# Kernel optimization log

Hardware: AMD Instinct MI355X
Metric: run time of the kernel (lower is better)

The kernel has to match this reference:

```python
import jax, jax.numpy as jnp
import numpy as np

L, D, H, FF, V = 8, 768, 8, 2048, 32000
MAXLEN, TMAX = 512, 4
S = MAXLEN * TMAX  # 2048 context length
HD = D // H
EPS = 1e-4  # layer_norm_eps from module defaults


def setup_inputs() -> dict:
    key = jax.random.key(0)
    ks = jax.random.split(key, 16)
    s = 0.02
    B = 1
    rn = lambda k, shape: jax.random.normal(k, shape, jnp.float32) * s
    # sinusoidal positional encoding over MAXLEN real-token positions
    pos = np.arange(MAXLEN)[:, None]
    div = np.exp(np.arange(0, D, 2) * (-np.log(10000.0) / D))
    pe = np.zeros((MAXLEN, D), np.float32)
    pe[:, 0::2] = np.sin(pos * div)
    pe[:, 1::2] = np.cos(pos * div)
    return {
        "state_embeddings": jax.random.normal(ks[0], (B, S, D), jnp.float32),
        "padding_mask": jnp.zeros((B, S), bool),
        "pe": jnp.asarray(pe),
        "thought_emb": rn(ks[1], (TMAX, D)),
        "w_qkv": rn(ks[2], (L, 3 * D, D)),
        "b_qkv": jnp.zeros((L, 3 * D), jnp.float32),
        "w_out": rn(ks[3], (L, D, D)),
        "b_out": jnp.zeros((L, D), jnp.float32),
        "ln1_g": jnp.ones((L, D), jnp.float32),
        "ln1_b": jnp.zeros((L, D), jnp.float32),
        "ln2_g": jnp.ones((L, D), jnp.float32),
        "ln2_b": jnp.zeros((L, D), jnp.float32),
        "w_ff1": rn(ks[4], (L, FF, D)),
        "b_ff1": jnp.zeros((L, FF), jnp.float32),
        "w_ff2": rn(ks[5], (L, D, FF)),
        "b_ff2": jnp.zeros((L, D), jnp.float32),
        "fn_g": jnp.ones((D,), jnp.float32),
        "fn_b": jnp.zeros((D,), jnp.float32),
        "w_policy": rn(ks[6], (V, D)),
        "w_v1": rn(ks[7], (FF, D)),
        "b_v1": jnp.zeros((FF,), jnp.float32),
        "w_v2": rn(ks[8], (1, FF)),
        "b_v2": jnp.zeros((1,), jnp.float32),
        "n_thoughts_taken": 3,
    }


def _layer_norm(x, g, b):
    m = x.mean(-1, keepdims=True)
    v = ((x - m) ** 2).mean(-1, keepdims=True)
    return (x - m) / jnp.sqrt(v + EPS) * g + b


def reference(state_embeddings, padding_mask, pe, thought_emb, w_qkv, b_qkv, w_out, b_out, ln1_g, ln1_b, ln2_g, ln2_b, w_ff1, b_ff1, w_ff2, b_ff2, fn_g, fn_b, w_policy, w_v1, b_v1, w_v2, b_v2, n_thoughts_taken):
    tt = int(n_thoughts_taken)
    T = tt + 1  # block size (token + thoughts taken)
    B = state_embeddings.shape[0]
    R = MAXLEN  # real_token_count: all token slots real (no padding)
    # --- DualPositionalEncoding ---
    x = state_embeddings[:, :MAXLEN * T].reshape(B, MAXLEN, T, D)
    x = x + pe[None, :, None, :] + thought_emb[None, None, :T, :]
    x = x.reshape(B, MAXLEN * T, D)
    x = jnp.pad(x, ((0, 0), (0, S - MAXLEN * T), (0, 0)))
    # --- ThoughtsFormer block-causal mask (keep=True means attend) ---
    i = jnp.arange(S)
    tok, off = i // T, i % T
    same_block = (tok[:, None] == tok[None, :]) & (off[:, None] >= off[None, :]) & (tok[:, None] < R)
    global_cols = (off[None, :] == 0) & (tok[None, :] < R) & (i[:, None] > i[None, :]) & (i[:, None] < R * T)
    keep = (same_block | global_cols)[None, None] & (~padding_mask)[:, None, None, :]
    scale = 1.0 / np.sqrt(HD)

    def layer(h, p):
        wq, bq, wo, bo, g1, b1, g2, b2, wf1, bf1, wf2, bf2 = p
        # pre-norm self-attention
        y = _layer_norm(h, g1, b1)
        q, k, v = jnp.split(y @ wq.T + bq, 3, axis=-1)
        q = q.reshape(B, S, H, HD)
        k = k.reshape(B, S, H, HD)
        v = v.reshape(B, S, H, HD)
        scores = jnp.einsum('bihd,bjhd->bhij', q, k) * scale
        attn = jax.nn.softmax(jnp.where(keep, scores, -jnp.inf), axis=-1)
        o = jnp.einsum('bhij,bjhd->bihd', attn, v).reshape(B, S, D)
        h = h + o @ wo.T + bo
        # pre-norm FFN with exact (erf) GELU
        y = _layer_norm(h, g2, b2)
        h = h + jax.nn.gelu(y @ wf1.T + bf1, approximate=False) @ wf2.T + bf2
        h = jnp.where(jnp.isnan(h), 0.0, h)
        return h, None

    x, _ = jax.lax.scan(layer, x, (w_qkv, b_qkv, w_out, b_out, ln1_g, ln1_b, ln2_g, ln2_b, w_ff1, b_ff1, w_ff2, b_ff2))
    x = _layer_norm(x, fn_g, fn_b)  # TransformerEncoder final norm
    logits = x @ w_policy.T  # policy head (no bias)
    values = jax.nn.gelu(x @ w_v1.T + b_v1, approximate=False) @ w_v2.T + b_v2
    return logits, values
```

## Files before the change

kernel.cpp:

```cpp
#include <hip/hip_runtime.h>
#include <math.h>

#define S_TOT 2048
#define DMODEL 768
#define QKVD 2304
#define NHEAD 8
#define HDIM 96
#define FFDIM 2048
#define VOCAB 32000
#define MAXLEN_C 512
#define POL_CHUNK 3200
#define VLT_LD 2080
#define NEG_BIG (-3.0e38f)
#define M_INIT (-1.0e30f)
#define QK_SCALE 0.10206207261596575f

typedef __bf16 bf16x8 __attribute__((ext_vector_type(8)));
typedef float f32x4 __attribute__((ext_vector_type(4)));
typedef unsigned short u16x8 __attribute__((ext_vector_type(8)));
typedef unsigned short u16x4 __attribute__((ext_vector_type(4)));

__device__ __forceinline__ float gelu_exact(float x) {
  return 0.5f * x * (1.0f + erff(x * 0.70710678118654752f));
}

__device__ __forceinline__ float bf2f(unsigned short u) {
  union { unsigned int i; float f; } v;
  v.i = ((unsigned int)u) << 16;
  return v.f;
}

__device__ __forceinline__ unsigned short f2bf(float f) {
  union { float f; unsigned int i; } v;
  v.f = f;
  unsigned int x = v.i;
  return (unsigned short)((x + 0x7fffu + ((x >> 16) & 1u)) >> 16);
}

__device__ __forceinline__ unsigned int pack2bf(float a, float b) {
  return (unsigned int)f2bf(a) | ((unsigned int)f2bf(b) << 16);
}

__device__ __forceinline__ void gload_lds16(const unsigned short* g, unsigned short* l) {
  __builtin_amdgcn_global_load_lds(
      (const __attribute__((address_space(1))) unsigned int*)g,
      (__attribute__((address_space(3))) unsigned int*)l, 16, 0, 0);
}

__global__ __launch_bounds__(256) void embed_kernel(
    const float* __restrict__ se, const float* __restrict__ pe,
    const float* __restrict__ th, const int* __restrict__ ntt,
    float* __restrict__ X) {
  int idx = blockIdx.x * 256 + threadIdx.x;
  if (idx >= S_TOT * DMODEL) return;
  int p = idx / DMODEL;
  int d = idx - p * DMODEL;
  int T = ntt[0] + 1;
  float v = 0.0f;
  if (p < MAXLEN_C * T) {
    v = se[idx] + pe[(p / T) * DMODEL + d] + th[(p % T) * DMODEL + d];
  }
  X[idx] = v;
}

__global__ __launch_bounds__(256) void ln_bf_kernel(
    const float* __restrict__ X, const float* __restrict__ g,
    const float* __restrict__ b, unsigned short* __restrict__ Y) {
  __shared__ float red[4];
  const int row = blockIdx.x;
  const int tid = threadIdx.x;
  const float* x = X + (size_t)row * DMODEL;
  float v0 = x[tid], v1 = x[tid + 256], v2 = x[tid + 512];
  float s = v0 + v1 + v2;
  for (int o = 32; o; o >>= 1) s += __shfl_xor(s, o);
  if ((tid & 63) == 0) red[tid >> 6] = s;
  __syncthreads();
  float mean = (red[0] + red[1] + red[2] + red[3]) * (1.0f / DMODEL);
  float d0 = v0 - mean, d1 = v1 - mean, d2 = v2 - mean;
  float s2 = d0 * d0 + d1 * d1 + d2 * d2;
  for (int o = 32; o; o >>= 1) s2 += __shfl_xor(s2, o);
  __syncthreads();
  if ((tid & 63) == 0) red[tid >> 6] = s2;
  __syncthreads();
  float var = (red[0] + red[1] + red[2] + red[3]) * (1.0f / DMODEL);
  float rstd = rsqrtf(var + 1e-4f);
  unsigned short* y = Y + (size_t)row * DMODEL;
  y[tid]       = f2bf(d0 * rstd * g[tid]       + b[tid]);
  y[tid + 256] = f2bf(d1 * rstd * g[tid + 256] + b[tid + 256]);
  y[tid + 512] = f2bf(d2 * rstd * g[tid + 512] + b[tid + 512]);
}

__global__ __launch_bounds__(256) void cvt_kernel(
    const float* __restrict__ s, unsigned short* __restrict__ d, int n) {
  int i = (blockIdx.x * 256 + threadIdx.x) * 4;
  if (i >= n) return;
  float4 v = *(const float4*)(s + i);
  u16x4 o;
  o[0] = f2bf(v.x); o[1] = f2bf(v.y); o[2] = f2bf(v.z); o[3] = f2bf(v.w);
  *(u16x4*)(d + i) = o;
}

__global__ __launch_bounds__(256) void cvt4_kernel(
    const float* __restrict__ s0, const float* __restrict__ s1,
    const float* __restrict__ s2, const float* __restrict__ s3,
    unsigned short* __restrict__ d0, unsigned short* __restrict__ d1,
    unsigned short* __restrict__ d2, unsigned short* __restrict__ d3,
    int n0, int n1, int n2, int n3) {
  int i = (blockIdx.x * 256 + threadIdx.x) * 4;
  const float* s;
  unsigned short* d;
  if (i < n0) { s = s0; d = d0; }
  else if (i < n0 + n1) { i -= n0; s = s1; d = d1; }
  else if (i < n0 + n1 + n2) { i -= n0 + n1; s = s2; d = d2; }
  else if (i < n0 + n1 + n2 + n3) { i -= n0 + n1 + n2; s = s3; d = d3; }
  else return;
  float4 v = *(const float4*)(s + i);
  u16x4 o;
  o[0] = f2bf(v.x); o[1] = f2bf(v.y); o[2] = f2bf(v.z); o[3] = f2bf(v.w);
  *(u16x4*)(d + i) = o;
}

__global__ __launch_bounds__(256) void cvt6_kernel(
    const float* __restrict__ s0, const float* __restrict__ s1,
    const float* __restrict__ s2, const float* __restrict__ s3,
    const float* __restrict__ s4, const float* __restrict__ s5,
    unsigned short* __restrict__ d0, unsigned short* __restrict__ d1,
    unsigned short* __restrict__ d2, unsigned short* __restrict__ d3,
    unsigned short* __restrict__ d4, unsigned short* __restrict__ d5,
    int n0, int n1, int n2, int n3, int n4, int n5) {
  int i = (blockIdx.x * 256 + threadIdx.x) * 4;
  const float* s;
  unsigned short* d;
  if (i < n0) { s = s0; d = d0; }
  else if (i < n0 + n1) { i -= n0; s = s1; d = d1; }
  else if (i < n0 + n1 + n2) { i -= n0 + n1; s = s2; d = d2; }
  else if (i < n0 + n1 + n2 + n3) { i -= n0 + n1 + n2; s = s3; d = d3; }
  else if (i < n0 + n1 + n2 + n3 + n4) { i -= n0 + n1 + n2 + n3; s = s4; d = d4; }
  else if (i < n0 + n1 + n2 + n3 + n4 + n5) { i -= n0 + n1 + n2 + n3 + n4; s = s5; d = d5; }
  else return;
  float4 v = *(const float4*)(s + i);
  u16x4 o;
  o[0] = f2bf(v.x); o[1] = f2bf(v.y); o[2] = f2bf(v.z); o[3] = f2bf(v.w);
  *(u16x4*)(d + i) = o;
}

__global__ __launch_bounds__(256) void gemm_bf16_kernel(
    const unsigned short* __restrict__ A, const unsigned short* __restrict__ B,
    const float* __restrict__ bias, const float* __restrict__ res,
    void* __restrict__ Cout, int M, int N, int K, int ldc, int act, int outbf,
    int swiz) {
  __shared__ __align__(16) unsigned short As[3 * 4096];
  __shared__ __align__(16) unsigned short Bs[3 * 4096];
  const int t = threadIdx.x;
  const int w = t >> 6, l = t & 63;
  int n_blk, m_blk;
  if (swiz) {
    const int g = blockIdx.x;
    const int chunk = gridDim.x >> 3;
    const int logical = (g & 7) * chunk + (g >> 3);
    m_blk = logical & 15;
    n_blk = logical >> 4;
  } else {
    n_blk = blockIdx.x; m_blk = blockIdx.y;
  }
  const int n0 = n_blk * 128, i0 = m_blk * 128;
  const int wr = w >> 1, wc = w & 1;
  const int lr = l & 15;
  const int koff = (l >> 4) * 8;

  f32x4 acc[4][4] = {};

  const int srow = t >> 2;
  const int scol = (t & 3) * 8;
  const unsigned short* Ag = A + (size_t)(i0 + srow) * K + scol;
  const unsigned short* Bg = B + (size_t)(n0 + srow) * K + scol;
  const int lo0 = (w << 9);
  const int lo1 = 2048 + (w << 9);

#define STAGE128(buf, k0)                                        \
  do {                                                           \
    gload_lds16(Ag + (k0), &As[(buf) * 4096 + lo0]);             \
    gload_lds16(Ag + (size_t)64 * K + (k0), &As[(buf) * 4096 + lo1]); \
    gload_lds16(Bg + (k0), &Bs[(buf) * 4096 + lo0]);             \
    gload_lds16(Bg + (size_t)64 * K + (k0), &Bs[(buf) * 4096 + lo1]); \
  } while (0)

#define COMPUTE128(buf)                                                   \
  do {                                                                    \
    const unsigned short* Ab = &As[(buf) * 4096];                         \
    const unsigned short* Bb = &Bs[(buf) * 4096];                         \
    bf16x8 af[4], bfr[4];                                                 \
    _Pragma("unroll") for (int fi = 0; fi < 4; ++fi)                      \
        af[fi] = *(const bf16x8*)&Ab[(wr * 64 + fi * 16 + lr) * 32 + koff]; \
    _Pragma("unroll") for (int fj = 0; fj < 4; ++fj)                      \
        bfr[fj] = *(const bf16x8*)&Bb[(wc * 64 + fj * 16 + lr) * 32 + koff]; \
    _Pragma("unroll") for (int fi = 0; fi < 4; ++fi)                      \
      _Pragma("unroll") for (int fj = 0; fj < 4; ++fj)                    \
          acc[fi][fj] = __builtin_amdgcn_mfma_f32_16x16x32_bf16(          \
              bfr[fj], af[fi], acc[fi][fj], 0, 0, 0);                     \
  } while (0)

  const int nt = K >> 5;
  STAGE128(0, 0);
  if (nt > 1) STAGE128(1, 32);
  for (int tt = 0; tt < nt; ++tt) {
    const int cb = tt % 3;
    if (tt + 2 < nt) {
      STAGE128((tt + 2) % 3, (tt + 2) << 5);
      asm volatile("s_waitcnt vmcnt(8)" ::: "memory");
    } else if (tt + 1 < nt) {
      asm volatile("s_waitcnt vmcnt(4)" ::: "memory");
    } else {
      asm volatile("s_waitcnt vmcnt(0)" ::: "memory");
    }
    __builtin_amdgcn_s_barrier();
    __builtin_amdgcn_sched_barrier(0);
    COMPUTE128(cb);
    __builtin_amdgcn_sched_barrier(0);
    __builtin_amdgcn_s_barrier();
  }

  const int mloc = l & 15, ng = (l >> 4) * 4;
#pragma unroll
  for (int fi = 0; fi < 4; ++fi) {
    const int i = i0 + wr * 64 + fi * 16 + mloc;
    const size_t rowbase = (size_t)i * ldc;
#pragma unroll
    for (int fj = 0; fj < 4; ++fj) {
      const int nb = n0 + wc * 64 + fj * 16 + ng;
      float z0 = acc[fi][fj][0], z1 = acc[fi][fj][1];
      float z2 = acc[fi][fj][2], z3 = acc[fi][fj][3];
      if (bias) {
        float4 bv = *(const float4*)(bias + nb);
        z0 += bv.x; z1 += bv.y; z2 += bv.z; z3 += bv.w;
      }
      if (act) {
        z0 = gelu_exact(z0); z1 = gelu_exact(z1);
        z2 = gelu_exact(z2); z3 = gelu_exact(z3);
      }
      if (res) {
        float4 rv = *(const float4*)(res + rowbase + nb);
        z0 += rv.x; z1 += rv.y; z2 += rv.z; z3 += rv.w;
      }
      if (outbf) {
        u16x4 o;
        o[0] = f2bf(z0); o[1] = f2bf(z1); o[2] = f2bf(z2); o[3] = f2bf(z3);
        *(u16x4*)((unsigned short*)Cout + rowbase + nb) = o;
      } else {
        *(float4*)((float*)Cout + rowbase + nb) = make_float4(z0, z1, z2, z3);
      }
    }
  }
#undef STAGE128
#undef COMPUTE128
}

__global__ __launch_bounds__(512) void gemm256_bf16_kernel(
    const unsigned short* __restrict__ A, const unsigned short* __restrict__ B,
    void* __restrict__ Cout, int M, int N, int K, int ldc) {
  __shared__ __align__(16) unsigned short As[2 * 8192];
  __shared__ __align__(16) unsigned short Bs[2 * 4096];
  const int t = threadIdx.x;
  const int w = t >> 6, l = t & 63;
  const int g = blockIdx.x;
  const int chunk = gridDim.x >> 3;
  const int logical = (g & 7) * chunk + (g >> 3);
  const int m_blk = logical & 7;
  const int n_blk = logical >> 3;
  const int n0 = n_blk * 128, i0 = m_blk * 256;
  const int wr = w >> 1;
  const int wc = w & 1;
  const int lr = l & 15;
  const int koff = (l >> 4) * 8;

  f32x4 acc[4][4] = {};

  const int srow = t >> 2;
  const int scol = (t & 3) * 8;
  const unsigned short* Ag = A + (size_t)(i0 + srow) * K + scol;
  const unsigned short* Bg = B + (size_t)(n0 + srow) * K + scol;
  const int lo = (w << 9);

#define STAGE256(buf, k0)                                             \
  do {                                                                \
    gload_lds16(Ag + (k0), &As[(buf) * 8192 + lo]);                   \
    gload_lds16(Ag + (size_t)128 * K + (k0), &As[(buf) * 8192 + 4096 + lo]); \
    gload_lds16(Bg + (k0), &Bs[(buf) * 4096 + lo]);                   \
  } while (0)

  const int nt = K >> 5;
  STAGE256(0, 0);
  for (int tt = 0; tt < nt; ++tt) {
    const int cb = tt & 1;
    if (tt + 1 < nt) {
      STAGE256(cb ^ 1, (tt + 1) << 5);
      asm volatile("s_waitcnt vmcnt(3)" ::: "memory");
    } else {
      asm volatile("s_waitcnt vmcnt(0)" ::: "memory");
    }
    __builtin_amdgcn_s_barrier();
    __builtin_amdgcn_sched_barrier(0);
    {
      const unsigned short* Ab = &As[cb * 8192];
      const unsigned short* Bb = &Bs[cb * 4096];
      bf16x8 af[4], bfr[4];
#pragma unroll
      for (int fi = 0; fi < 4; ++fi)
        af[fi] = *(const bf16x8*)&Ab[(wr * 64 + fi * 16 + lr) * 32 + koff];
#pragma unroll
      for (int fj = 0; fj < 4; ++fj)
        bfr[fj] = *(const bf16x8*)&Bb[(wc * 64 + fj * 16 + lr) * 32 + koff];
#pragma unroll
      for (int fi = 0; fi < 4; ++fi)
#pragma unroll
        for (int fj = 0; fj < 4; ++fj)
          acc[fi][fj] = __builtin_amdgcn_mfma_f32_16x16x32_bf16(
              bfr[fj], af[fi], acc[fi][fj], 0, 0, 0);
    }
    __builtin_amdgcn_sched_barrier(0);
    __builtin_amdgcn_s_barrier();
  }

  const int mloc = l & 15, ng = (l >> 4) * 4;
#pragma unroll
  for (int fi = 0; fi < 4; ++fi) {
    const int i = i0 + wr * 64 + fi * 16 + mloc;
    const size_t rowbase = (size_t)i * ldc;
#pragma unroll
    for (int fj = 0; fj < 4; ++fj) {
      const int nb = n0 + wc * 64 + fj * 16 + ng;
      *(float4*)((float*)Cout + rowbase + nb) =
          make_float4(acc[fi][fj][0], acc[fi][fj][1], acc[fi][fj][2], acc[fi][fj][3]);
    }
  }
#undef STAGE256
}

__global__ __launch_bounds__(256) void gemm64_bf16_kernel(
    const unsigned short* __restrict__ A, const unsigned short* __restrict__ B,
    const float* __restrict__ bias, const float* __restrict__ res,
    void* __restrict__ Cout, int M, int N, int K, int ldc, int act, int outbf) {
  __shared__ __align__(16) unsigned short As[3 * 4096];
  __shared__ __align__(16) unsigned short Bs[3 * 4096];
  const int t = threadIdx.x;
  const int w = t >> 6, l = t & 63;
  const int n0 = blockIdx.x * 64, i0 = blockIdx.y * 64;
  const int wr = w >> 1, wc = w & 1;
  const int lr = l & 15;
  const int koff = (l >> 4) * 8;

  f32x4 acc[2][2] = {};

  const int srow = t >> 2;
  const int scol = (t & 3) * 8;
  const unsigned short* Ag = A + (size_t)(i0 + srow) * K + scol;
  const unsigned short* Bg = B + (size_t)(n0 + srow) * K + scol;
  const int lo0 = (w << 9);
  const int lo1 = 2048 + (w << 9);

#define STAGE64(buf, k0)                                      \
  do {                                                        \
    gload_lds16(Ag + (k0), &As[(buf) * 4096 + lo0]);          \
    gload_lds16(Ag + (k0) + 32, &As[(buf) * 4096 + lo1]);     \
    gload_lds16(Bg + (k0), &Bs[(buf) * 4096 + lo0]);          \
    gload_lds16(Bg + (k0) + 32, &Bs[(buf) * 4096 + lo1]);     \
  } while (0)

#define COMPUTE64(buf)                                                        \
  do {                                                                        \
    const unsigned short* Ab = &As[(buf) * 4096];                             \
    const unsigned short* Bb = &Bs[(buf) * 4096];                             \
    bf16x8 af[2][2], bfr[2][2];                                               \
    _Pragma("unroll") for (int fi = 0; fi < 2; ++fi)                          \
      _Pragma("unroll") for (int kk = 0; kk < 2; ++kk)                        \
          af[fi][kk] = *(const bf16x8*)&Ab[kk * 2048 + (wr * 32 + fi * 16 + lr) * 32 + koff]; \
    _Pragma("unroll") for (int fj = 0; fj < 2; ++fj)                          \
      _Pragma("unroll") for (int kk = 0; kk < 2; ++kk)                        \
          bfr[fj][kk] = *(const bf16x8*)&Bb[kk * 2048 + (wc * 32 + fj * 16 + lr) * 32 + koff]; \
    _Pragma("unroll") for (int fi = 0; fi < 2; ++fi)                          \
      _Pragma("unroll") for (int fj = 0; fj < 2; ++fj)                        \
        _Pragma("unroll") for (int kk = 0; kk < 2; ++kk)                      \
            acc[fi][fj] = __builtin_amdgcn_mfma_f32_16x16x32_bf16(            \
                bfr[fj][kk], af[fi][kk], acc[fi][fj], 0, 0, 0);               \
  } while (0)

  const int nt = K >> 6;
  STAGE64(0, 0);
  if (nt > 1) STAGE64(1, 64);
  for (int tt = 0; tt < nt; ++tt) {
    const int cb = tt % 3;
    if (tt + 2 < nt) {
      STAGE64((tt + 2) % 3, (tt + 2) << 6);
      asm volatile("s_waitcnt vmcnt(8)" ::: "memory");
    } else if (tt + 1 < nt) {
      asm volatile("s_waitcnt vmcnt(4)" ::: "memory");
    } else {
      asm volatile("s_waitcnt vmcnt(0)" ::: "memory");
    }
    __builtin_amdgcn_s_barrier();
    __builtin_amdgcn_sched_barrier(0);
    COMPUTE64(cb);
    __builtin_amdgcn_sched_barrier(0);
    __builtin_amdgcn_s_barrier();
  }

  const int mloc = l & 15, ng = (l >> 4) * 4;
#pragma unroll
  for (int fi = 0; fi < 2; ++fi) {
    const int i = i0 + wr * 32 + fi * 16 + mloc;
    const size_t rowbase = (size_t)i * ldc;
#pragma unroll
    for (int fj = 0; fj < 2; ++fj) {
      const int nb = n0 + wc * 32 + fj * 16 + ng;
      float z0 = acc[fi][fj][0], z1 = acc[fi][fj][1];
      float z2 = acc[fi][fj][2], z3 = acc[fi][fj][3];
      if (bias) {
        float4 bv = *(const float4*)(bias + nb);
        z0 += bv.x; z1 += bv.y; z2 += bv.z; z3 += bv.w;
      }
      if (act) {
        z0 = gelu_exact(z0); z1 = gelu_exact(z1);
        z2 = gelu_exact(z2); z3 = gelu_exact(z3);
      }
      if (res) {
        float4 rv = *(const float4*)(res + rowbase + nb);
        z0 += rv.x; z1 += rv.y; z2 += rv.z; z3 += rv.w;
      }
      if (outbf) {
        u16x4 o;
        o[0] = f2bf(z0); o[1] = f2bf(z1); o[2] = f2bf(z2); o[3] = f2bf(z3);
        *(u16x4*)((unsigned short*)Cout + rowbase + nb) = o;
      } else {
        *(float4*)((float*)Cout + rowbase + nb) = make_float4(z0, z1, z2, z3);
      }
    }
  }
#undef STAGE64
#undef COMPUTE64
}

__global__ __launch_bounds__(256) void repack_kernel(
    const unsigned short* __restrict__ qkv, const int* __restrict__ ntt,
    unsigned short* __restrict__ Kg, unsigned short* __restrict__ Vgt,
    unsigned short* __restrict__ Vlt) {
  __shared__ unsigned short vt[64][104];
  const int pb = blockIdx.x * 64, h = blockIdx.y;
  const int T = ntt[0] + 1;
  const int tid = threadIdx.x;

  for (int idx = tid; idx < 64 * 96; idx += 256) {
    int pp = idx / 96, d = idx - pp * 96;
    vt[pp][d] = qkv[(size_t)(pb + pp) * QKVD + 2 * DMODEL + h * HDIM + d];
  }
  const int firstpp = (T - pb % T) % T;
  const int ng = (64 - firstpp + T - 1) / T;
  for (int idx = tid; idx < ng * 96; idx += 256) {
    int gi = idx / 96, d = idx - gi * 96;
    int p = pb + firstpp + gi * T;
    int g = p / T;
    if (g < MAXLEN_C)
      Kg[((size_t)h * 512 + g) * 96 + d] = qkv[(size_t)p * QKVD + DMODEL + h * HDIM + d];
  }
  __syncthreads();
  for (int idx = tid; idx < 96 * 64; idx += 256) {
    int d = idx >> 6, pp = idx & 63;
    Vlt[((size_t)h * 96 + d) * VLT_LD + pb + pp] = vt[pp][d];
  }
  for (int idx = tid; idx < ng * 96; idx += 256) {
    int d = idx / ng, gi = idx - d * ng;
    int pp = firstpp + gi * T;
    int g = (pb + pp) / T;
    if (g < MAXLEN_C && d < 96)
      Vgt[((size_t)h * 96 + d) * 512 + g] = vt[pp][d];
  }
}

__global__ __launch_bounds__(256) void attn_flash_kernel(
    const unsigned short* __restrict__ qkv, const unsigned short* __restrict__ Kg,
    const unsigned short* __restrict__ Vgt, const unsigned short* __restrict__ Vlt,
    const int* __restrict__ ntt, unsigned short* __restrict__ att) {
  __shared__ float Osh[4][96][17];
  __shared__ float Msh[4][16];
  __shared__ float Lsh[4][16];
  const int s = blockIdx.x, h = blockIdx.y;
  const int T = ntt[0] + 1;
  const int tid = threadIdx.x;
  const int w = tid >> 6, l = tid & 63;
  const int q15 = l & 15, grp = l >> 4;
  const int p0 = s * 16;
  const int p = p0 + q15;
  const int myTok = p / T;

  const unsigned short* qrow = qkv + (size_t)p * QKVD + h * HDIM + grp * 8;
  bf16x8 qf0 = *(const bf16x8*)(qrow);
  bf16x8 qf1 = *(const bf16x8*)(qrow + 32);
  bf16x8 qf2 = *(const bf16x8*)(qrow + 64);

  float m_run = M_INIT, l_run = 0.0f;
  f32x4 oacc[6] = {};

  const int gmax = (p0 + 15) / T;
  const int KP = (gmax >> 5) + 1;
  const unsigned short* KgH = Kg + (size_t)h * 512 * 96;
  const unsigned short* VgH = Vgt + (size_t)h * 96 * 512;

  for (int kp = w; kp < KP; kp += 4) {
    f32x4 s0 = {}, s1 = {};
    const unsigned short* k0r = KgH + (size_t)(kp * 32 + q15) * 96 + grp * 8;
    const unsigned short* k1r = k0r + 16 * 96;
    {
      bf16x8 a0 = *(const bf16x8*)(k0r);
      bf16x8 a1 = *(const bf16x8*)(k1r);
      bf16x8 b0 = *(const bf16x8*)(k0r + 32);
      bf16x8 b1 = *(const bf16x8*)(k1r + 32);
      bf16x8 c0 = *(const bf16x8*)(k0r + 64);
      bf16x8 c1 = *(const bf16x8*)(k1r + 64);
      __builtin_amdgcn_s_setprio(1);
      s0 = __builtin_amdgcn_mfma_f32_16x16x32_bf16(a0, qf0, s0, 0, 0, 0);
      s1 = __builtin_amdgcn_mfma_f32_16x16x32_bf16(a1, qf0, s1, 0, 0, 0);
      s0 = __builtin_amdgcn_mfma_f32_16x16x32_bf16(b0, qf1, s0, 0, 0, 0);
      s1 = __builtin_amdgcn_mfma_f32_16x16x32_bf16(b1, qf1, s1, 0, 0, 0);
      s0 = __builtin_amdgcn_mfma_f32_16x16x32_bf16(c0, qf2, s0, 0, 0, 0);
      s1 = __builtin_amdgcn_mfma_f32_16x16x32_bf16(c1, qf2, s1, 0, 0, 0);
      __builtin_amdgcn_s_setprio(0);
    }
    float sc[8];
#pragma unroll
    for (int e = 0; e < 4; ++e) {
      int g = kp * 32 + grp * 4 + e;
      sc[e] = (g * T <= p) ? s0[e] * QK_SCALE : NEG_BIG;
      g += 16;
      sc[4 + e] = (g * T <= p) ? s1[e] * QK_SCALE : NEG_BIG;
    }
    float tmax = sc[0];
#pragma unroll
    for (int e = 1; e < 8; ++e) tmax = fmaxf(tmax, sc[e]);
    tmax = fmaxf(tmax, __shfl_xor(tmax, 16));
    tmax = fmaxf(tmax, __shfl_xor(tmax, 32));
    float mnew = fmaxf(m_run, tmax);
    float alpha = __expf(m_run - mnew);
    float pv[8], ps = 0.0f;
#pragma unroll
    for (int e = 0; e < 8; ++e) { pv[e] = __expf(sc[e] - mnew); ps += pv[e]; }
    ps += __shfl_xor(ps, 16);
    ps += __shfl_xor(ps, 32);
    l_run = l_run * alpha + ps;
    m_run = mnew;
#pragma unroll
    for (int dt = 0; dt < 6; ++dt) oacc[dt] *= alpha;
    unsigned int pk0[2], pk1[2];
    pk0[0] = pack2bf(pv[0], pv[1]); pk0[1] = pack2bf(pv[2], pv[3]);
    pk1[0] = pack2bf(pv[4], pv[5]); pk1[1] = pack2bf(pv[6], pv[7]);
    union { unsigned int u[4]; bf16x8 v; } pf;
#pragma unroll
    for (int w2 = 0; w2 < 4; ++w2) {
      int src = (((grp & 1) << 1) + (w2 >> 1)) * 16 + q15;
      int y0 = __shfl((int)pk0[w2 & 1], src);
      int y1 = __shfl((int)pk1[w2 & 1], src);
      pf.u[w2] = (grp >> 1) ? (unsigned int)y1 : (unsigned int)y0;
    }
    __builtin_amdgcn_s_setprio(1);
#pragma unroll
    for (int dt = 0; dt < 6; ++dt) {
      bf16x8 vf = *(const bf16x8*)(VgH + (size_t)(dt * 16 + q15) * 512 + kp * 32 + grp * 8);
      oacc[dt] = __builtin_amdgcn_mfma_f32_16x16x32_bf16(vf, pf.v, oacc[dt], 0, 0, 0);
    }
    __builtin_amdgcn_s_setprio(0);
  }

  if (w == 3) {
    f32x4 s0 = {};
    const unsigned short* kl = qkv + (size_t)(p0 + q15) * QKVD + DMODEL + h * HDIM + grp * 8;
    __builtin_amdgcn_s_setprio(1);
    s0 = __builtin_amdgcn_mfma_f32_16x16x32_bf16(*(const bf16x8*)(kl), qf0, s0, 0, 0, 0);
    s0 = __builtin_amdgcn_mfma_f32_16x16x32_bf16(*(const bf16x8*)(kl + 32), qf1, s0, 0, 0, 0);
    s0 = __builtin_amdgcn_mfma_f32_16x16x32_bf16(*(const bf16x8*)(kl + 64), qf2, s0, 0, 0, 0);
    __builtin_amdgcn_s_setprio(0);
    float sc[4];
#pragma unroll
    for (int e = 0; e < 4; ++e) {
      int pk = p0 + grp * 4 + e;
      bool ok = (pk / T == myTok) && (pk % T != 0) && (pk <= p);
      sc[e] = ok ? s0[e] * QK_SCALE : NEG_BIG;
    }
    float tmax = fmaxf(fmaxf(sc[0], sc[1]), fmaxf(sc[2], sc[3]));
    tmax = fmaxf(tmax, __shfl_xor(tmax, 16));
    tmax = fmaxf(tmax, __shfl_xor(tmax, 32));
    float mnew = fmaxf(m_run, tmax);
    float alpha = __expf(m_run - mnew);
    float pv[4], ps = 0.0f;
#pragma unroll
    for (int e = 0; e < 4; ++e) { pv[e] = __expf(sc[e] - mnew); ps += pv[e]; }
    ps += __shfl_xor(ps, 16);
    ps += __shfl_xor(ps, 32);
    l_run = l_run * alpha + ps;
    m_run = mnew;
#pragma unroll
    for (int dt = 0; dt < 6; ++dt) oacc[dt] *= alpha;
    unsigned int pk0[2];
    pk0[0] = pack2bf(pv[0], pv[1]); pk0[1] = pack2bf(pv[2], pv[3]);
    union { unsigned int u[4]; bf16x8 v; } pf;
#pragma unroll
    for (int w2 = 0; w2 < 4; ++w2) {
      int src = (((grp & 1) << 1) + (w2 >> 1)) * 16 + q15;
      int y0 = __shfl((int)pk0[w2 & 1], src);
      pf.u[w2] = (grp >> 1) ? 0u : (unsigned int)y0;
    }
    __builtin_amdgcn_s_setprio(1);
#pragma unroll
    for (int dt = 0; dt < 6; ++dt) {
      bf16x8 vf = *(const bf16x8*)(Vlt + ((size_t)h * 96 + dt * 16 + q15) * VLT_LD + p0 + grp * 8);
      oacc[dt] = __builtin_amdgcn_mfma_f32_16x16x32_bf16(vf, pf.v, oacc[dt], 0, 0, 0);
    }
    __builtin_amdgcn_s_setprio(0);
  }

  if (l < 16) { Msh[w][l] = m_run; Lsh[w][l] = l_run; }
#pragma unroll
  for (int dt = 0; dt < 6; ++dt)
#pragma unroll
    for (int e = 0; e < 4; ++e)
      Osh[w][dt * 16 + grp * 4 + e][q15] = oacc[dt][e];
  __syncthreads();

  {
    const int q = tid & 15, dg = tid >> 4;
    float m0 = Msh[0][q], m1 = Msh[1][q], m2 = Msh[2][q], m3 = Msh[3][q];
    float ms = fmaxf(fmaxf(m0, m1), fmaxf(m2, m3));
    float c0 = __expf(m0 - ms), c1 = __expf(m1 - ms);
    float c2 = __expf(m2 - ms), c3 = __expf(m3 - ms);
    float lsum = c0 * Lsh[0][q] + c1 * Lsh[1][q] + c2 * Lsh[2][q] + c3 * Lsh[3][q];
    float rinv = 1.0f / lsum;
    unsigned short* orow = att + (size_t)(p0 + q) * DMODEL + h * HDIM;
#pragma unroll
    for (int j = 0; j < 6; ++j) {
      int d = dg * 6 + j;
      float o = c0 * Osh[0][d][q] + c1 * Osh[1][d][q] +
                c2 * Osh[2][d][q] + c3 * Osh[3][d][q];
      orow[d] = f2bf(o * rinv);
    }
  }
}

__global__ __launch_bounds__(256) void v2_kernel(
    const unsigned short* __restrict__ F1, const float* __restrict__ w2,
    const float* __restrict__ b2, float* __restrict__ out) {
  __shared__ float red[4];
  const int row = blockIdx.x;
  const int tid = threadIdx.x;
  float s = 0.0f;
  const unsigned short* xr = F1 + (size_t)row * FFDIM;
  for (int f = tid; f < FFDIM; f += 256) s += bf2f(xr[f]) * w2[f];
  for (int o = 32; o; o >>= 1) s += __shfl_xor(s, o);
  if ((tid & 63) == 0) red[tid >> 6] = s;
  __syncthreads();
  if (tid == 0) out[row] = red[0] + red[1] + red[2] + red[3] + b2[0];
}

extern "C" void kernel_launch(void* const* d_in, const int* in_sizes, int n_in,
                              void* d_out, int out_size, void* d_ws, size_t ws_size,
                              hipStream_t stream) {
  const float* se      = (const float*)d_in[0];
  const float* pe      = (const float*)d_in[2];
  const float* th      = (const float*)d_in[3];
  const float* w_qkv   = (const float*)d_in[4];
  const float* b_qkv   = (const float*)d_in[5];
  const float* w_out   = (const float*)d_in[6];
  const float* b_out   = (const float*)d_in[7];
  const float* ln1_g   = (const float*)d_in[8];
  const float* ln1_b   = (const float*)d_in[9];
  const float* ln2_g   = (const float*)d_in[10];
  const float* ln2_b   = (const float*)d_in[11];
  const float* w_ff1   = (const float*)d_in[12];
  const float* b_ff1   = (const float*)d_in[13];
  const float* w_ff2   = (const float*)d_in[14];
  const float* b_ff2   = (const float*)d_in[15];
  const float* fn_g    = (const float*)d_in[16];
  const float* fn_b    = (const float*)d_in[17];
  const float* w_pol   = (const float*)d_in[18];
  const float* w_v1    = (const float*)d_in[19];
  const float* b_v1    = (const float*)d_in[20];
  const float* w_v2    = (const float*)d_in[21];
  const float* b_v2    = (const float*)d_in[22];
  const int*   ntt     = (const int*)d_in[23];

  float* logits = (float*)d_out;
  float* values = logits + (size_t)S_TOT * VOCAB;

  const int nq = 3 * DMODEL * DMODEL, no = DMODEL * DMODEL;
  const int nf1 = FFDIM * DMODEL, nf2 = DMODEL * FFDIM;
  const int npol = VOCAB * DMODEL;

  char* p = (char*)d_ws;
  float* X             = (float*)p;          p += (size_t)S_TOT * DMODEL * 4;
  unsigned short* Ybf  = (unsigned short*)p; p += (size_t)S_TOT * DMODEL * 2;
  unsigned short* QKVb = (unsigned short*)p; p += (size_t)S_TOT * QKVD * 2;
  unsigned short* ATTb = (unsigned short*)p; p += (size_t)S_TOT * DMODEL * 2;
  unsigned short* F1b  = (unsigned short*)p; p += (size_t)S_TOT * FFDIM * 2;
  unsigned short* Kg   = (unsigned short*)p; p += (size_t)NHEAD * 512 * 96 * 2;
  unsigned short* Vgt  = (unsigned short*)p; p += (size_t)NHEAD * 96 * 512 * 2;
  unsigned short* Vlt  = (unsigned short*)p; p += (size_t)NHEAD * 96 * VLT_LD * 2;

  const size_t wbytes = ((size_t)8 * (nq + no + nf1 + nf2) + npol + nf1) * 2;
  const size_t used   = (size_t)(p - (char*)d_ws);
  const bool bigws = ws_size >= used + wbytes + (1u << 20);

  unsigned short *WqA, *WoA, *Wf1A, *Wf2A, *WpolA, *Wv1A;
  if (bigws) {
    WqA   = (unsigned short*)p; p += (size_t)8 * nq * 2;
    WoA   = (unsigned short*)p; p += (size_t)8 * no * 2;
    Wf1A  = (unsigned short*)p; p += (size_t)8 * nf1 * 2;
    Wf2A  = (unsigned short*)p; p += (size_t)8 * nf2 * 2;
    WpolA = (unsigned short*)p; p += (size_t)npol * 2;
    Wv1A  = (unsigned short*)p;
  } else {
    WqA   = (unsigned short*)p; p += (size_t)nq * 2;
    WoA   = (unsigned short*)p; p += (size_t)no * 2;
    Wf1A  = (unsigned short*)p; p += (size_t)nf1 * 2;
    Wf2A  = (unsigned short*)p; p += (size_t)nf2 * 2;
    WpolA = (unsigned short*)p;
    Wv1A  = Wf1A;
  }

  dim3 blk(256);

  if (bigws) {
    const int t0 = 8 * nq, t1 = 8 * no, t2 = 8 * nf1, t3 = 8 * nf2;
    const long total = (long)t0 + t1 + t2 + t3 + npol + nf1;
    cvt6_kernel<<<dim3((unsigned)((total / 4 + 255) / 256)), blk, 0, stream>>>(
        w_qkv, w_out, w_ff1, w_ff2, w_pol, w_v1,
        WqA, WoA, Wf1A, Wf2A, WpolA, Wv1A,
        t0, t1, t2, t3, npol, nf1);
  }

  embed_kernel<<<dim3((S_TOT * DMODEL + 255) / 256), blk, 0, stream>>>(se, pe, th, ntt, X);

  for (int l = 0; l < 8; ++l) {
    const unsigned short* pWq  = bigws ? WqA  + (size_t)l * nq  : WqA;
    const unsigned short* pWo  = bigws ? WoA  + (size_t)l * no  : WoA;
    const unsigned short* pWf1 = bigws ? Wf1A + (size_t)l * nf1 : Wf1A;
    const unsigned short* pWf2 = bigws ? Wf2A + (size_t)l * nf2 : Wf2A;
    if (!bigws) {
      const int ncvt4 = (nq + no + nf1 + nf2) / 4;
      cvt4_kernel<<<dim3((ncvt4 + 255) / 256), blk, 0, stream>>>(
          w_qkv + (size_t)l * nq, w_out + (size_t)l * no,
          w_ff1 + (size_t)l * nf1, w_ff2 + (size_t)l * nf2,
          WqA, WoA, Wf1A, Wf2A, nq, no, nf1, nf2);
    }

    ln_bf_kernel<<<dim3(S_TOT), blk, 0, stream>>>(X, ln1_g + l * DMODEL, ln1_b + l * DMODEL, Ybf);
    gemm64_bf16_kernel<<<dim3(QKVD / 64, S_TOT / 64), blk, 0, stream>>>(
        Ybf, pWq, b_qkv + (size_t)l * 3 * DMODEL, nullptr, QKVb,
        S_TOT, QKVD, DMODEL, QKVD, 0, 1);
    repack_kernel<<<dim3(S_TOT / 64, NHEAD), blk, 0, stream>>>(QKVb, ntt, Kg, Vgt, Vlt);
    attn_flash_kernel<<<dim3(S_TOT / 16, NHEAD), blk, 0, stream>>>(
        QKVb, Kg, Vgt, Vlt, ntt, ATTb);
    gemm64_bf16_kernel<<<dim3(DMODEL / 64, S_TOT / 64), blk, 0, stream>>>(
        ATTb, pWo, b_out + (size_t)l * DMODEL, X, X,
        S_TOT, DMODEL, DMODEL, DMODEL, 0, 0);

    ln_bf_kernel<<<dim3(S_TOT), blk, 0, stream>>>(X, ln2_g + l * DMODEL, ln2_b + l * DMODEL, Ybf);
    gemm64_bf16_kernel<<<dim3(FFDIM / 64, S_TOT / 64), blk, 0, stream>>>(
        Ybf, pWf1, b_ff1 + (size_t)l * FFDIM, nullptr, F1b,
        S_TOT, FFDIM, DMODEL, FFDIM, 1, 1);
    gemm64_bf16_kernel<<<dim3(DMODEL / 64, S_TOT / 64), blk, 0, stream>>>(
        F1b, pWf2, b_ff2 + (size_t)l * DMODEL, X, X,
        S_TOT, DMODEL, FFDIM, DMODEL, 0, 0);
  }

  ln_bf_kernel<<<dim3(S_TOT), blk, 0, stream>>>(X, fn_g, fn_b, Ybf);

  if (bigws) {
    gemm256_bf16_kernel<<<dim3((S_TOT / 256) * (VOCAB / 128)), dim3(512), 0, stream>>>(
        Ybf, WpolA, logits, S_TOT, VOCAB, DMODEL, VOCAB);
  } else {
    for (int c = 0; c < VOCAB / POL_CHUNK; ++c) {
      cvt_kernel<<<dim3((POL_CHUNK * DMODEL / 4 + 255) / 256), blk, 0, stream>>>(
          w_pol + (size_t)c * POL_CHUNK * DMODEL, WpolA, POL_CHUNK * DMODEL);
      gemm_bf16_kernel<<<dim3(POL_CHUNK / 128, S_TOT / 128), blk, 0, stream>>>(
          Ybf, WpolA, nullptr, nullptr, logits + (size_t)c * POL_CHUNK,
          S_TOT, POL_CHUNK, DMODEL, VOCAB, 0, 0, 0);
    }
  }

  if (!bigws)
    cvt_kernel<<<dim3((nf1 / 4 + 255) / 256), blk, 0, stream>>>(w_v1, Wv1A, nf1);
  gemm64_bf16_kernel<<<dim3(FFDIM / 64, S_TOT / 64), blk, 0, stream>>>(
      Ybf, Wv1A, b_v1, nullptr, F1b, S_TOT, FFDIM, DMODEL, FFDIM, 1, 1);
  v2_kernel<<<dim3(S_TOT), blk, 0, stream>>>(F1b, w_v2, b_v2, values);
}
```

Measured before the change: 1.347 ms.

## Fuse K/V repack into QKV GEMM epilogue and drop a barrier per k-step

Removes the separate repack kernel by having the QKV GEMM epilogue write the gathered K, transposed V, and transposed gathered V buffers directly. It also cuts the GEMM main loops from two workgroup barriers per k-iteration to one, relying on the triple-buffered LDS to avoid overwrite hazards. The fused epilogue does scattered 2-byte strided stores for the V transposes, which may be less coalesced than the old LDS-staged transpose.

Result: faster. 1.292 ms (-4.0%).

```diff
diff --git a/kernel.cpp b/kernel.cpp
--- a/kernel.cpp
+++ b/kernel.cpp
@@ -204,7 +204,7 @@
   STAGE128(0, 0);
   if (nt > 1) STAGE128(1, 32);
   for (int tt = 0; tt < nt; ++tt) {
-    const int cb = tt % 3;
+    __builtin_amdgcn_s_barrier();
     if (tt + 2 < nt) {
       STAGE128((tt + 2) % 3, (tt + 2) << 5);
       asm volatile("s_waitcnt vmcnt(8)" ::: "memory");
@@ -213,11 +213,9 @@
     } else {
       asm volatile("s_waitcnt vmcnt(0)" ::: "memory");
     }
-    __builtin_amdgcn_s_barrier();
     __builtin_amdgcn_sched_barrier(0);
-    COMPUTE128(cb);
+    COMPUTE128(tt % 3);
     __builtin_amdgcn_sched_barrier(0);
-    __builtin_amdgcn_s_barrier();
   }
 
   const int mloc = l & 15, ng = (l >> 4) * 4;
@@ -339,7 +337,9 @@
 __global__ __launch_bounds__(256) void gemm64_bf16_kernel(
     const unsigned short* __restrict__ A, const unsigned short* __restrict__ B,
     const float* __restrict__ bias, const float* __restrict__ res,
-    void* __restrict__ Cout, int M, int N, int K, int ldc, int act, int outbf) {
+    void* __restrict__ Cout, int M, int N, int K, int ldc, int act, int outbf,
+    const int* __restrict__ ntt, unsigned short* __restrict__ Kg,
+    unsigned short* __restrict__ Vgt, unsigned short* __restrict__ Vlt) {
   __shared__ __align__(16) unsigned short As[3 * 4096];
   __shared__ __align__(16) unsigned short Bs[3 * 4096];
   const int t = threadIdx.x;
@@ -348,6 +348,7 @@
   const int wr = w >> 1, wc = w & 1;
   const int lr = l & 15;
   const int koff = (l >> 4) * 8;
+  const int T = Kg ? (ntt[0] + 1) : 1;
 
   f32x4 acc[2][2] = {};
 
@@ -388,7 +389,7 @@
   STAGE64(0, 0);
   if (nt > 1) STAGE64(1, 64);
   for (int tt = 0; tt < nt; ++tt) {
-    const int cb = tt % 3;
+    __builtin_amdgcn_s_barrier();
     if (tt + 2 < nt) {
       STAGE64((tt + 2) % 3, (tt + 2) << 6);
       asm volatile("s_waitcnt vmcnt(8)" ::: "memory");
@@ -397,11 +398,9 @@
     } else {
       asm volatile("s_waitcnt vmcnt(0)" ::: "memory");
     }
-    __builtin_amdgcn_s_barrier();
     __builtin_amdgcn_sched_barrier(0);
-    COMPUTE64(cb);
+    COMPUTE64(tt % 3);
     __builtin_amdgcn_sched_barrier(0);
-    __builtin_amdgcn_s_barrier();
   }
 
   const int mloc = l & 15, ng = (l >> 4) * 4;
@@ -430,6 +429,34 @@
         u16x4 o;
         o[0] = f2bf(z0); o[1] = f2bf(z1); o[2] = f2bf(z2); o[3] = f2bf(z3);
         *(u16x4*)((unsigned short*)Cout + rowbase + nb) = o;
+        if (Kg) {
+          if (nb >= DMODEL && nb < 2 * DMODEL) {
+            if (i % T == 0) {
+              const int gg = i / T;
+              if (gg < MAXLEN_C) {
+                const int kcol = nb - DMODEL;
+                const int h = kcol / HDIM, d = kcol - h * HDIM;
+                *(u16x4*)&Kg[((size_t)h * 512 + gg) * HDIM + d] = o;
+              }
+            }
+          } else if (nb >= 2 * DMODEL) {
+            const int vcol = nb - 2 * DMODEL;
+            const int h = vcol / HDIM, d = vcol - h * HDIM;
+            Vlt[((size_t)h * HDIM + d + 0) * VLT_LD + i] = o[0];
+            Vlt[((size_t)h * HDIM + d + 1) * VLT_LD + i] = o[1];
+            Vlt[((size_t)h * HDIM + d + 2) * VLT_LD + i] = o[2];
+            Vlt[((size_t)h * HDIM + d + 3) * VLT_LD + i] = o[3];
+            if (i % T == 0) {
+              const int gg = i / T;
+              if (gg < MAXLEN_C) {
+                Vgt[((size_t)h * HDIM + d + 0) * 512 + gg] = o[0];
+                Vgt[((size_t)h * HDIM + d + 1) * 512 + gg] = o[1];
+                Vgt[((size_t)h * HDIM + d + 2) * 512 + gg] = o[2];
+                Vgt[((size_t)h * HDIM + d + 3) * 512 + gg] = o[3];
+              }
+            }
+          }
+        }
       } else {
         *(float4*)((float*)Cout + rowbase + nb) = make_float4(z0, z1, z2, z3);
       }
@@ -437,42 +464,6 @@
   }
 #undef STAGE64
 #undef COMPUTE64
-}
-
-__global__ __launch_bounds__(256) void repack_kernel(
-    const unsigned short* __restrict__ qkv, const int* __restrict__ ntt,
-    unsigned short* __restrict__ Kg, unsigned short* __restrict__ Vgt,
-    unsigned short* __restrict__ Vlt) {
-  __shared__ unsigned short vt[64][104];
-  const int pb = blockIdx.x * 64, h = blockIdx.y;
-  const int T = ntt[0] + 1;
-  const int tid = threadIdx.x;
-
-  for (int idx = tid; idx < 64 * 96; idx += 256) {
-    int pp = idx / 96, d = idx - pp * 96;
-    vt[pp][d] = qkv[(size_t)(pb + pp) * QKVD + 2 * DMODEL + h * HDIM + d];
-  }
-  const int firstpp = (T - pb % T) % T;
-  const int ng = (64 - firstpp + T - 1) / T;
-  for (int idx = tid; idx < ng * 96; idx += 256) {
-    int gi = idx / 96, d = idx - gi * 96;
-    int p = pb + firstpp + gi * T;
-    int g = p / T;
-    if (g < MAXLEN_C)
-      Kg[((size_t)h * 512 + g) * 96 + d] = qkv[(size_t)p * QKVD + DMODEL + h * HDIM + d];
-  }
-  __syncthreads();
-  for (int idx = tid; idx < 96 * 64; idx += 256) {
-    int d = idx >> 6, pp = idx & 63;
-    Vlt[((size_t)h * 96 + d) * VLT_LD + pb + pp] = vt[pp][d];
-  }
-  for (int idx = tid; idx < ng * 96; idx += 256) {
-    int d = idx / ng, gi = idx - d * ng;
-    int pp = firstpp + gi * T;
-    int g = (pb + pp) / T;
-    if (g < MAXLEN_C && d < 96)
-      Vgt[((size_t)h * 96 + d) * 512 + g] = vt[pp][d];
-  }
 }
 
 __global__ __launch_bounds__(256) void attn_flash_kernel(
@@ -751,21 +742,20 @@
     ln_bf_kernel<<<dim3(S_TOT), blk, 0, stream>>>(X, ln1_g + l * DMODEL, ln1_b + l * DMODEL, Ybf);
     gemm64_bf16_kernel<<<dim3(QKVD / 64, S_TOT / 64), blk, 0, stream>>>(
         Ybf, pWq, b_qkv + (size_t)l * 3 * DMODEL, nullptr, QKVb,
-        S_TOT, QKVD, DMODEL, QKVD, 0, 1);
-    repack_kernel<<<dim3(S_TOT / 64, NHEAD), blk, 0, stream>>>(QKVb, ntt, Kg, Vgt, Vlt);
+        S_TOT, QKVD, DMODEL, QKVD, 0, 1, ntt, Kg, Vgt, Vlt);
     attn_flash_kernel<<<dim3(S_TOT / 16, NHEAD), blk, 0, stream>>>(
         QKVb, Kg, Vgt, Vlt, ntt, ATTb);
     gemm64_bf16_kernel<<<dim3(DMODEL / 64, S_TOT / 64), blk, 0, stream>>>(
         ATTb, pWo, b_out + (size_t)l * DMODEL, X, X,
-        S_TOT, DMODEL, DMODEL, DMODEL, 0, 0);
+        S_TOT, DMODEL, DMODEL, DMODEL, 0, 0, nullptr, nullptr, nullptr, nullptr);
 
     ln_bf_kernel<<<dim3(S_TOT), blk, 0, stream>>>(X, ln2_g + l * DMODEL, ln2_b + l * DMODEL, Ybf);
     gemm64_bf16_kernel<<<dim3(FFDIM / 64, S_TOT / 64), blk, 0, stream>>>(
         Ybf, pWf1, b_ff1 + (size_t)l * FFDIM, nullptr, F1b,
-        S_TOT, FFDIM, DMODEL, FFDIM, 1, 1);
+        S_TOT, FFDIM, DMODEL, FFDIM, 1, 1, nullptr, nullptr, nullptr, nullptr);
     gemm64_bf16_kernel<<<dim3(DMODEL / 64, S_TOT / 64), blk, 0, stream>>>(
         F1b, pWf2, b_ff2 + (size_t)l * DMODEL, X, X,
-        S_TOT, DMODEL, FFDIM, DMODEL, 0, 0);
+        S_TOT, DMODEL, FFDIM, DMODEL, 0, 0, nullptr, nullptr, nullptr, nullptr);
   }
 
   ln_bf_kernel<<<dim3(S_TOT), blk, 0, stream>>>(X, fn_g, fn_b, Ybf);
@@ -786,6 +776,7 @@
   if (!bigws)
     cvt_kernel<<<dim3((nf1 / 4 + 255) / 256), blk, 0, stream>>>(w_v1, Wv1A, nf1);
   gemm64_bf16_kernel<<<dim3(FFDIM / 64, S_TOT / 64), blk, 0, stream>>>(
-      Ybf, Wv1A, b_v1, nullptr, F1b, S_TOT, FFDIM, DMODEL, FFDIM, 1, 1);
+      Ybf, Wv1A, b_v1, nullptr, F1b, S_TOT, FFDIM, DMODEL, FFDIM, 1, 1,
+      nullptr, nullptr, nullptr, nullptr);
   v2_kernel<<<dim3(S_TOT), blk, 0, stream>>>(F1b, w_v2, b_v2, values);
 }
```
